# Kernel tuning notes

Measured on AMD Instinct MI355X. Metric: run time of the kernel, lower is better.

The kernel has to match this reference:

```python
import jax, jax.numpy as jnp
import numpy as np

N = 50000   # num nodes
D = 64      # feature dim
R = 4       # num relations (len(adjs))
E = 800000  # edges per relation (avg degree 16)


def setup_inputs() -> dict:
    key = jax.random.key(0)
    k0, k1, k2, k3, k4 = jax.random.split(key, 5)
    x = jax.random.normal(k0, (N, D), dtype=jnp.float32)
    weight = jax.random.normal(k1, (R,), dtype=jnp.float32)        # scalar weight per relation
    edge_vals = jax.random.uniform(k2, (R, E), dtype=jnp.float32)  # nonzero values of adjs
    edge_rows = jax.random.randint(k3, (R, E), 0, N)               # COO row (destination) indices
    edge_cols = jax.random.randint(k4, (R, E), 0, N)               # COO col (source) indices
    return {"x": x, "weight": weight, "edge_vals": edge_vals,
            "edge_rows": edge_rows, "edge_cols": edge_cols, "idx": 1}


def reference(x, weight, edge_vals, edge_rows, edge_cols, idx):
    # spmm(adjs[idx], x): gather source features, scale by edge values, scatter-add to rows
    rows = edge_rows[idx]
    cols = edge_cols[idx]
    vals = edge_vals[idx]
    msgs = vals[:, None] * x[cols]                                  # [E, D]
    agg = jax.ops.segment_sum(msgs, rows, num_segments=N)           # [N, D]
    return weight[idx] * agg
```

## Files before the change

kernel.cpp:

```cpp
#include <hip/hip_runtime.h>


#define FEAT_D 64
#define BROWS 32
#define BSH 5
#define LCAP 40
#define OVFCAP 16384
#define EPB 8192
#define BBLOCK 512
#define GBLOCK 512

__global__ void build_kernel(const float* __restrict__ edge_vals,
                             const int* __restrict__ edge_rows,
                             const int* __restrict__ edge_cols,
                             const int* __restrict__ idx_ptr,
                             int* __restrict__ bktcnt,
                             int2* __restrict__ pack,
                             int* __restrict__ ovfcnt,
                             int4* __restrict__ ovfbuf,
                             int E, int NBKT, int cap) {
    extern __shared__ int lh[];
    const long long off = (long long)idx_ptr[0] * E;
    const int* rows = edge_rows + off;
    const int* cols = edge_cols + off;
    const float* vals = edge_vals + off;
    for (int k = threadIdx.x; k < NBKT; k += blockDim.x) lh[k] = 0;
    __syncthreads();
    const int s = blockIdx.x * EPB;
    const int e2 = min(s + EPB, E);
    for (int g = s + threadIdx.x; g < e2; g += blockDim.x)
        atomicAdd(&lh[rows[g] >> BSH], 1);
    __syncthreads();
    for (int k = threadIdx.x; k < NBKT; k += blockDim.x) {
        const int c = lh[k];
        if (c) lh[k] = atomicAdd(&bktcnt[k], c);
    }
    __syncthreads();
    for (int g = s + threadIdx.x; g < e2; g += blockDim.x) {
        const int r = rows[g], c = cols[g];
        const int b = r >> BSH;
        const int pos = atomicAdd(&lh[b], 1);
        if (pos < cap) {
            pack[(long long)b * cap + pos] =
                make_int2((c << BSH) | (r & (BROWS - 1)), __float_as_int(vals[g]));
        } else {
            const int o = atomicAdd(ovfcnt, 1);
            if (o < OVFCAP) ovfbuf[o] = make_int4(r, c, __float_as_int(vals[g]), 0);
        }
    }
}

__global__ __launch_bounds__(GBLOCK) void gather_kernel(
        const float* __restrict__ x,
        const float* __restrict__ weight,
        const int* __restrict__ idx_ptr,
        const int* __restrict__ bktcnt,
        const int2* __restrict__ pack,
        int* __restrict__ ovfcnt, int4* __restrict__ ovfbuf,
        float* __restrict__ out, int N, int cap) {
    extern __shared__ int2 sh2[];
    int2* sraw = sh2;
    int2* slist = sh2 + cap;
    __shared__ int scur[32];
    const int b = blockIdx.x;
    const int t = threadIdx.x;
    const int w = t >> 6;
    const int lane = t & 63;
    if (t < 32) scur[t] = 0;
    const int cnt = min(bktcnt[b], cap);
    for (int i = t; i < cnt; i += GBLOCK)
        sraw[i] = pack[(long long)b * cap + i];
    __syncthreads();
    for (int j = lane; j < cnt; j += 64) {
        const int2 rec = sraw[j];
        const int rl = rec.x & (BROWS - 1);
        if ((rl >> 2) == w) {
            const int q = rl & 3;
            const int li = atomicAdd(&scur[w * 4 + q], 1);
            if (li < LCAP) {
                slist[(w * 4 + q) * LCAP + li] = rec;
            } else {
                const int o = atomicAdd(ovfcnt, 1);
                const int row = (b << BSH) | rl;
                if (o < OVFCAP) ovfbuf[o] = make_int4(row, rec.x >> BSH, rec.y, 0);
            }
        }
    }
    __syncthreads();
    const float wscale = weight[idx_ptr[0]];
    const int base = w * 4;
    float acc0 = 0.f, acc1 = 0.f, acc2 = 0.f, acc3 = 0.f;
#define ROWACC(Q, ACC)                                                        \
    {                                                                         \
        const int n = min(scur[base + Q], LCAP);                              \
        const int2* lp = slist + (base + Q) * LCAP;                           \
        int j = 0;                                                            \
        for (; j + 4 <= n; j += 4) {                                          \
            const int2 r0 = lp[j], r1 = lp[j + 1], r2 = lp[j + 2],            \
                       r3 = lp[j + 3];                                        \
            const float x0 = x[(r0.x >> BSH) * FEAT_D + lane];                \
            const float x1 = x[(r1.x >> BSH) * FEAT_D + lane];                \
            const float x2 = x[(r2.x >> BSH) * FEAT_D + lane];                \
            const float x3 = x[(r3.x >> BSH) * FEAT_D + lane];                \
            ACC += __int_as_float(r0.y) * x0 + __int_as_float(r1.y) * x1 +    \
                   __int_as_float(r2.y) * x2 + __int_as_float(r3.y) * x3;     \
        }                                                                     \
        for (; j < n; ++j) {                                                  \
            const int2 r0 = lp[j];                                            \
            ACC += __int_as_float(r0.y) * x[(r0.x >> BSH) * FEAT_D + lane];   \
        }                                                                     \
    }
    ROWACC(0, acc0)
    ROWACC(1, acc1)
    ROWACC(2, acc2)
    ROWACC(3, acc3)
#undef ROWACC
    const int row0 = (b << BSH) + base;
    if (row0 + 0 < N) out[(long long)(row0 + 0) * FEAT_D + lane] = wscale * acc0;
    if (row0 + 1 < N) out[(long long)(row0 + 1) * FEAT_D + lane] = wscale * acc1;
    if (row0 + 2 < N) out[(long long)(row0 + 2) * FEAT_D + lane] = wscale * acc2;
    if (row0 + 3 < N) out[(long long)(row0 + 3) * FEAT_D + lane] = wscale * acc3;
}

__global__ void fixup_kernel(const float* __restrict__ x,
                             const float* __restrict__ weight,
                             const int* __restrict__ idx_ptr,
                             const int* __restrict__ ovfcnt,
                             const int4* __restrict__ ovfbuf,
                             float* __restrict__ out) {
    const int n = min(*ovfcnt, OVFCAP);
    if (n == 0) return;
    const float ws = weight[idx_ptr[0]];
    const int gw = (int)((blockIdx.x * (long long)blockDim.x + threadIdx.x) >> 6);
    const int lane = threadIdx.x & 63;
    const int nw = (gridDim.x * blockDim.x) >> 6;
    for (int r = gw; r < n; r += nw) {
        const int4 rec = ovfbuf[r];
        atomicAdd(&out[(long long)rec.x * FEAT_D + lane],
                  ws * __int_as_float(rec.z) * x[(long long)rec.y * FEAT_D + lane]);
    }
}

__global__ void spmm_scatter_kernel(const float* __restrict__ x,
                                    const float* __restrict__ weight,
                                    const float* __restrict__ edge_vals,
                                    const int* __restrict__ edge_rows,
                                    const int* __restrict__ edge_cols,
                                    const int* __restrict__ idx_ptr,
                                    float* __restrict__ out,
                                    int E, long long work) {
    const int idx = idx_ptr[0];
    const float w = weight[idx];
    const long long rel_off = (long long)idx * E;
    long long t = (long long)blockIdx.x * blockDim.x + threadIdx.x;
    if (t >= work) return;
    const int e = (int)(t >> 4);
    const int q = (int)(t & 15);
    const int r = edge_rows[rel_off + e];
    const int c = edge_cols[rel_off + e];
    const float wv = w * edge_vals[rel_off + e];
    const float4 xv = *reinterpret_cast<const float4*>(x + (long long)c * FEAT_D + q * 4);
    float* op = out + (long long)r * FEAT_D + q * 4;
    atomicAdd(op + 0, wv * xv.x);
    atomicAdd(op + 1, wv * xv.y);
    atomicAdd(op + 2, wv * xv.z);
    atomicAdd(op + 3, wv * xv.w);
}

extern "C" void kernel_launch(void* const* d_in, const int* in_sizes, int n_in,
                              void* d_out, int out_size, void* d_ws, size_t ws_size,
                              hipStream_t stream) {
    const float* x         = (const float*)d_in[0];
    const float* weight    = (const float*)d_in[1];
    const float* edge_vals = (const float*)d_in[2];
    const int*   edge_rows = (const int*)d_in[3];
    const int*   edge_cols = (const int*)d_in[4];
    const int*   idx_ptr   = (const int*)d_in[5];
    float* out = (float*)d_out;

    const int R = in_sizes[1];
    const int E = in_sizes[2] / R;
    const int N = in_sizes[0] / FEAT_D;
    const int NBKT = (N + BROWS - 1) >> BSH;

    char* ws = (char*)d_ws;
    size_t o_bktcnt = 0;
    size_t o_ovfcnt = o_bktcnt + (size_t)NBKT * 4;
    size_t o_ovfbuf = ((o_ovfcnt + 4 + 15) / 16) * 16;
    size_t o_pack   = o_ovfbuf + (size_t)OVFCAP * 16;
    const size_t room = (ws_size > o_pack) ? (ws_size - o_pack) : 0;
    int cap = (int)(room / ((size_t)NBKT * 8));
    if (cap > 1024) cap = 1024;

    const long long meanload = (NBKT > 0) ? ((long long)E / NBKT) : 0;
    if (cap < 64 || cap < meanload + (meanload >> 3) + 16 || NBKT > 8192) {
        hipMemsetAsync(d_out, 0, (size_t)out_size * sizeof(float), stream);
        const long long work = (long long)E * 16;
        const int block = 256;
        const long long grid = (work + block - 1) / block;
        spmm_scatter_kernel<<<dim3((unsigned)grid), dim3(block), 0, stream>>>(
            x, weight, edge_vals, edge_rows, edge_cols, idx_ptr, out, E, work);
        return;
    }

    int*  bktcnt = (int*)(ws + o_bktcnt);
    int*  ovfcnt = (int*)(ws + o_ovfcnt);
    int4* ovfbuf = (int4*)(ws + o_ovfbuf);
    int2* pack   = (int2*)(ws + o_pack);

    hipMemsetAsync(bktcnt, 0, (size_t)NBKT * 4 + 4, stream);

    const int bgrid = (E + EPB - 1) / EPB;
    const size_t blds = (size_t)NBKT * 4;
    build_kernel<<<bgrid, BBLOCK, blds, stream>>>(edge_vals, edge_rows,
                                                  edge_cols, idx_ptr, bktcnt,
                                                  pack, ovfcnt, ovfbuf,
                                                  E, NBKT, cap);

    const size_t glds = ((size_t)cap + 32 * LCAP) * 8;
    gather_kernel<<<NBKT, GBLOCK, glds, stream>>>(x, weight, idx_ptr, bktcnt,
                                                  pack, ovfcnt, ovfbuf,
                                                  out, N, cap);

    fixup_kernel<<<64, 256, 0, stream>>>(x, weight, idx_ptr, ovfcnt, ovfbuf, out);
}
```

Baseline: 150.5 us.

## Bin gather-kernel edges by source-column range to improve x cache locality

Each warp's edges are now grouped by the high bits of the source column into four column ranges instead of by destination row. Each range is processed in turn with a block-wide barrier in between, so all warps touch the same slice of x at once and reuse it in cache. Rows are accumulated with predicated selects, the inner loop is unrolled to 8, and the pack loads and output stores use nontemporal hints. In exchange the kernel adds per-edge select overhead and extra barriers. It also sends N above 65536 to the fallback scatter path, and the per-list overflow cap is raised.

```diff
diff --git a/kernel.cpp b/kernel.cpp
--- a/kernel.cpp
+++ b/kernel.cpp
@@ -4,7 +4,9 @@
 #define FEAT_D 64
 #define BROWS 32
 #define BSH 5
-#define LCAP 40
+#define NCR 4
+#define CRSH 14
+#define LCAP 48
 #define OVFCAP 16384
 #define EPB 8192
 #define BBLOCK 512
@@ -61,24 +63,27 @@
     extern __shared__ int2 sh2[];
     int2* sraw = sh2;
     int2* slist = sh2 + cap;
-    __shared__ int scur[32];
+    __shared__ int scur[NCR * 8];
     const int b = blockIdx.x;
     const int t = threadIdx.x;
     const int w = t >> 6;
     const int lane = t & 63;
-    if (t < 32) scur[t] = 0;
+    if (t < NCR * 8) scur[t] = 0;
     const int cnt = min(bktcnt[b], cap);
-    for (int i = t; i < cnt; i += GBLOCK)
-        sraw[i] = pack[(long long)b * cap + i];
+    const long long* psrc = (const long long*)(pack + (long long)b * cap);
+    for (int i = t; i < cnt; i += GBLOCK) {
+        const long long raw = __builtin_nontemporal_load(psrc + i);
+        sraw[i] = make_int2((int)(unsigned)raw, (int)(raw >> 32));
+    }
     __syncthreads();
     for (int j = lane; j < cnt; j += 64) {
         const int2 rec = sraw[j];
         const int rl = rec.x & (BROWS - 1);
         if ((rl >> 2) == w) {
-            const int q = rl & 3;
-            const int li = atomicAdd(&scur[w * 4 + q], 1);
+            const int cr = rec.x >> (BSH + CRSH);
+            const int li = atomicAdd(&scur[cr * 8 + w], 1);
             if (li < LCAP) {
-                slist[(w * 4 + q) * LCAP + li] = rec;
+                slist[(cr * 8 + w) * LCAP + li] = rec;
             } else {
                 const int o = atomicAdd(ovfcnt, 1);
                 const int row = (b << BSH) | rl;
@@ -87,39 +92,62 @@
         }
     }
     __syncthreads();
-    const float wscale = weight[idx_ptr[0]];
-    const int base = w * 4;
     float acc0 = 0.f, acc1 = 0.f, acc2 = 0.f, acc3 = 0.f;
-#define ROWACC(Q, ACC)                                                        \
+#define EDGE(Rc, XV)                                                          \
     {                                                                         \
-        const int n = min(scur[base + Q], LCAP);                              \
-        const int2* lp = slist + (base + Q) * LCAP;                           \
-        int j = 0;                                                            \
-        for (; j + 4 <= n; j += 4) {                                          \
-            const int2 r0 = lp[j], r1 = lp[j + 1], r2 = lp[j + 2],            \
-                       r3 = lp[j + 3];                                        \
-            const float x0 = x[(r0.x >> BSH) * FEAT_D + lane];                \
-            const float x1 = x[(r1.x >> BSH) * FEAT_D + lane];                \
-            const float x2 = x[(r2.x >> BSH) * FEAT_D + lane];                \
-            const float x3 = x[(r3.x >> BSH) * FEAT_D + lane];                \
-            ACC += __int_as_float(r0.y) * x0 + __int_as_float(r1.y) * x1 +    \
-                   __int_as_float(r2.y) * x2 + __int_as_float(r3.y) * x3;     \
-        }                                                                     \
-        for (; j < n; ++j) {                                                  \
-            const int2 r0 = lp[j];                                            \
-            ACC += __int_as_float(r0.y) * x[(r0.x >> BSH) * FEAT_D + lane];   \
-        }                                                                     \
-    }
-    ROWACC(0, acc0)
-    ROWACC(1, acc1)
-    ROWACC(2, acc2)
-    ROWACC(3, acc3)
-#undef ROWACC
-    const int row0 = (b << BSH) + base;
-    if (row0 + 0 < N) out[(long long)(row0 + 0) * FEAT_D + lane] = wscale * acc0;
-    if (row0 + 1 < N) out[(long long)(row0 + 1) * FEAT_D + lane] = wscale * acc1;
-    if (row0 + 2 < N) out[(long long)(row0 + 2) * FEAT_D + lane] = wscale * acc2;
-    if (row0 + 3 < N) out[(long long)(row0 + 3) * FEAT_D + lane] = wscale * acc3;
+        const float m = __int_as_float(Rc.y) * XV;                            \
+        const int q = Rc.x & 3;                                               \
+        acc0 += (q == 0) ? m : 0.f;                                           \
+        acc1 += (q == 1) ? m : 0.f;                                           \
+        acc2 += (q == 2) ? m : 0.f;                                           \
+        acc3 += (q == 3) ? m : 0.f;                                           \
+    }
+    for (int cr = 0; cr < NCR; ++cr) {
+        const int li = cr * 8 + w;
+        const int n = min(scur[li], LCAP);
+        const int2* lp = slist + li * LCAP;
+        int j = 0;
+        for (; j + 8 <= n; j += 8) {
+            const int2 r0 = lp[j],     r1 = lp[j + 1], r2 = lp[j + 2],
+                       r3 = lp[j + 3], r4 = lp[j + 4], r5 = lp[j + 5],
+                       r6 = lp[j + 6], r7 = lp[j + 7];
+            const float x0 = x[(r0.x >> BSH) * FEAT_D + lane];
+            const float x1 = x[(r1.x >> BSH) * FEAT_D + lane];
+            const float x2 = x[(r2.x >> BSH) * FEAT_D + lane];
+            const float x3 = x[(r3.x >> BSH) * FEAT_D + lane];
+            const float x4 = x[(r4.x >> BSH) * FEAT_D + lane];
+            const float x5 = x[(r5.x >> BSH) * FEAT_D + lane];
+            const float x6 = x[(r6.x >> BSH) * FEAT_D + lane];
+            const float x7 = x[(r7.x >> BSH) * FEAT_D + lane];
+            EDGE(r0, x0) EDGE(r1, x1) EDGE(r2, x2) EDGE(r3, x3)
+            EDGE(r4, x4) EDGE(r5, x5) EDGE(r6, x6) EDGE(r7, x7)
+        }
+        for (; j + 4 <= n; j += 4) {
+            const int2 r0 = lp[j], r1 = lp[j + 1], r2 = lp[j + 2], r3 = lp[j + 3];
+            const float x0 = x[(r0.x >> BSH) * FEAT_D + lane];
+            const float x1 = x[(r1.x >> BSH) * FEAT_D + lane];
+            const float x2 = x[(r2.x >> BSH) * FEAT_D + lane];
+            const float x3 = x[(r3.x >> BSH) * FEAT_D + lane];
+            EDGE(r0, x0) EDGE(r1, x1) EDGE(r2, x2) EDGE(r3, x3)
+        }
+        for (; j < n; ++j) {
+            const int2 r0 = lp[j];
+            const float x0 = x[(r0.x >> BSH) * FEAT_D + lane];
+            EDGE(r0, x0)
+        }
+        __syncthreads();
+    }
+#undef EDGE
+    const float ws = weight[idx_ptr[0]];
+    const int row0 = (b << BSH) + w * 4;
+    if (row0 + 0 < N)
+        __builtin_nontemporal_store(ws * acc0, &out[(long long)(row0 + 0) * FEAT_D + lane]);
+    if (row0 + 1 < N)
+        __builtin_nontemporal_store(ws * acc1, &out[(long long)(row0 + 1) * FEAT_D + lane]);
+    if (row0 + 2 < N)
+        __builtin_nontemporal_store(ws * acc2, &out[(long long)(row0 + 2) * FEAT_D + lane]);
+    if (row0 + 3 < N)
+        __builtin_nontemporal_store(ws * acc3, &out[(long long)(row0 + 3) * FEAT_D + lane]);
 }
 
 __global__ void fixup_kernel(const float* __restrict__ x,
@@ -193,7 +221,8 @@
     if (cap > 1024) cap = 1024;
 
     const long long meanload = (NBKT > 0) ? ((long long)E / NBKT) : 0;
-    if (cap < 64 || cap < meanload + (meanload >> 3) + 16 || NBKT > 8192) {
+    if (cap < 64 || cap < meanload + (meanload >> 3) + 16 || NBKT > 8192 ||
+        N > (1 << (CRSH + 2))) {
         hipMemsetAsync(d_out, 0, (size_t)out_size * sizeof(float), stream);
         const long long work = (long long)E * 16;
         const int block = 256;
@@ -217,7 +246,7 @@
                                                   pack, ovfcnt, ovfbuf,
                                                   E, NBKT, cap);
 
-    const size_t glds = ((size_t)cap + 32 * LCAP) * 8;
+    const size_t glds = ((size_t)cap + NCR * 8 * LCAP) * 8;
     gather_kernel<<<NBKT, GBLOCK, glds, stream>>>(x, weight, idx_ptr, bktcnt,
                                                   pack, ovfcnt, ovfbuf,
                                                   out, N, cap);
```

Result: slower. 161.5 us (+7.3%).

## Stream bucket records directly into per-row lists and cache rows in build kernel

Applied to the files above, without the earlier changes.

The gather kernel no longer stages each bucket's raw records in shared memory and then rescans them per wavefront. All threads now read records once with nontemporal loads and scatter them straight into per-row lists with shared atomics. That cuts shared-memory use, drops the dynamic LDS allocation and removes one full pass over the bucket. The build kernel keeps row indices in registers between the histogram and scatter passes, halves edges per block for more blocks, and raises the per-row list cap. Output uses nontemporal stores. More contention on the per-row counters and more register pressure are the risks.

```diff
diff --git a/kernel.cpp b/kernel.cpp
--- a/kernel.cpp
+++ b/kernel.cpp
@@ -4,48 +4,64 @@
 #define FEAT_D 64
 #define BROWS 32
 #define BSH 5
-#define LCAP 40
+#define LCAP 48
 #define OVFCAP 16384
-#define EPB 8192
+#define EPB 4096
 #define BBLOCK 512
+#define EPT (EPB / BBLOCK)
 #define GBLOCK 512
 
-__global__ void build_kernel(const float* __restrict__ edge_vals,
-                             const int* __restrict__ edge_rows,
-                             const int* __restrict__ edge_cols,
-                             const int* __restrict__ idx_ptr,
-                             int* __restrict__ bktcnt,
-                             int2* __restrict__ pack,
-                             int* __restrict__ ovfcnt,
-                             int4* __restrict__ ovfbuf,
-                             int E, int NBKT, int cap) {
+__global__ __launch_bounds__(BBLOCK) void build_kernel(
+        const float* __restrict__ edge_vals,
+        const int* __restrict__ edge_rows,
+        const int* __restrict__ edge_cols,
+        const int* __restrict__ idx_ptr,
+        int* __restrict__ bktcnt,
+        int2* __restrict__ pack,
+        int* __restrict__ ovfcnt,
+        int4* __restrict__ ovfbuf,
+        int E, int NBKT, int cap) {
     extern __shared__ int lh[];
     const long long off = (long long)idx_ptr[0] * E;
     const int* rows = edge_rows + off;
     const int* cols = edge_cols + off;
     const float* vals = edge_vals + off;
-    for (int k = threadIdx.x; k < NBKT; k += blockDim.x) lh[k] = 0;
+    for (int k = threadIdx.x; k < NBKT; k += BBLOCK) lh[k] = 0;
     __syncthreads();
     const int s = blockIdx.x * EPB;
     const int e2 = min(s + EPB, E);
-    for (int g = s + threadIdx.x; g < e2; g += blockDim.x)
-        atomicAdd(&lh[rows[g] >> BSH], 1);
-    __syncthreads();
-    for (int k = threadIdx.x; k < NBKT; k += blockDim.x) {
+    int myrow[EPT];
+#pragma unroll
+    for (int k = 0; k < EPT; ++k) {
+        const int g = s + threadIdx.x + k * BBLOCK;
+        if (g < e2) {
+            const int r = rows[g];
+            myrow[k] = r;
+            atomicAdd(&lh[r >> BSH], 1);
+        }
+    }
+    __syncthreads();
+    for (int k = threadIdx.x; k < NBKT; k += BBLOCK) {
         const int c = lh[k];
         if (c) lh[k] = atomicAdd(&bktcnt[k], c);
     }
     __syncthreads();
-    for (int g = s + threadIdx.x; g < e2; g += blockDim.x) {
-        const int r = rows[g], c = cols[g];
-        const int b = r >> BSH;
-        const int pos = atomicAdd(&lh[b], 1);
-        if (pos < cap) {
-            pack[(long long)b * cap + pos] =
-                make_int2((c << BSH) | (r & (BROWS - 1)), __float_as_int(vals[g]));
-        } else {
-            const int o = atomicAdd(ovfcnt, 1);
-            if (o < OVFCAP) ovfbuf[o] = make_int4(r, c, __float_as_int(vals[g]), 0);
+#pragma unroll
+    for (int k = 0; k < EPT; ++k) {
+        const int g = s + threadIdx.x + k * BBLOCK;
+        if (g < e2) {
+            const int r = myrow[k];
+            const int b = r >> BSH;
+            const int c = cols[g];
+            const float v = vals[g];
+            const int pos = atomicAdd(&lh[b], 1);
+            if (pos < cap) {
+                pack[(long long)b * cap + pos] =
+                    make_int2((c << BSH) | (r & (BROWS - 1)), __float_as_int(v));
+            } else {
+                const int o = atomicAdd(ovfcnt, 1);
+                if (o < OVFCAP) ovfbuf[o] = make_int4(r, c, __float_as_int(v), 0);
+            }
         }
     }
 }
@@ -58,42 +74,37 @@
         const int2* __restrict__ pack,
         int* __restrict__ ovfcnt, int4* __restrict__ ovfbuf,
         float* __restrict__ out, int N, int cap) {
-    extern __shared__ int2 sh2[];
-    int2* sraw = sh2;
-    int2* slist = sh2 + cap;
-    __shared__ int scur[32];
+    __shared__ int2 slist[BROWS * LCAP];
+    __shared__ int scur[BROWS];
     const int b = blockIdx.x;
     const int t = threadIdx.x;
     const int w = t >> 6;
     const int lane = t & 63;
-    if (t < 32) scur[t] = 0;
+    if (t < BROWS) scur[t] = 0;
+    __syncthreads();
     const int cnt = min(bktcnt[b], cap);
-    for (int i = t; i < cnt; i += GBLOCK)
-        sraw[i] = pack[(long long)b * cap + i];
-    __syncthreads();
-    for (int j = lane; j < cnt; j += 64) {
-        const int2 rec = sraw[j];
+    const long long* psrc = (const long long*)(pack + (long long)b * cap);
+    for (int j = t; j < cnt; j += GBLOCK) {
+        const long long raw = __builtin_nontemporal_load(psrc + j);
+        const int2 rec = make_int2((int)(unsigned)raw, (int)(raw >> 32));
         const int rl = rec.x & (BROWS - 1);
-        if ((rl >> 2) == w) {
-            const int q = rl & 3;
-            const int li = atomicAdd(&scur[w * 4 + q], 1);
-            if (li < LCAP) {
-                slist[(w * 4 + q) * LCAP + li] = rec;
-            } else {
-                const int o = atomicAdd(ovfcnt, 1);
-                const int row = (b << BSH) | rl;
-                if (o < OVFCAP) ovfbuf[o] = make_int4(row, rec.x >> BSH, rec.y, 0);
-            }
+        const int li = atomicAdd(&scur[rl], 1);
+        if (li < LCAP) {
+            slist[rl * LCAP + li] = rec;
+        } else {
+            const int o = atomicAdd(ovfcnt, 1);
+            const int row = (b << BSH) | rl;
+            if (o < OVFCAP) ovfbuf[o] = make_int4(row, rec.x >> BSH, rec.y, 0);
         }
     }
     __syncthreads();
-    const float wscale = weight[idx_ptr[0]];
-    const int base = w * 4;
+    const float ws = weight[idx_ptr[0]];
     float acc0 = 0.f, acc1 = 0.f, acc2 = 0.f, acc3 = 0.f;
 #define ROWACC(Q, ACC)                                                        \
     {                                                                         \
-        const int n = min(scur[base + Q], LCAP);                              \
-        const int2* lp = slist + (base + Q) * LCAP;                           \
+        const int rl = w * 4 + Q;                                             \
+        const int n = min(scur[rl], LCAP);                                    \
+        const int2* lp = slist + rl * LCAP;                                   \
         int j = 0;                                                            \
         for (; j + 4 <= n; j += 4) {                                          \
             const int2 r0 = lp[j], r1 = lp[j + 1], r2 = lp[j + 2],            \
@@ -115,11 +126,15 @@
     ROWACC(2, acc2)
     ROWACC(3, acc3)
 #undef ROWACC
-    const int row0 = (b << BSH) + base;
-    if (row0 + 0 < N) out[(long long)(row0 + 0) * FEAT_D + lane] = wscale * acc0;
-    if (row0 + 1 < N) out[(long long)(row0 + 1) * FEAT_D + lane] = wscale * acc1;
-    if (row0 + 2 < N) out[(long long)(row0 + 2) * FEAT_D + lane] = wscale * acc2;
-    if (row0 + 3 < N) out[(long long)(row0 + 3) * FEAT_D + lane] = wscale * acc3;
+    const int row0 = (b << BSH) + w * 4;
+    if (row0 + 0 < N)
+        __builtin_nontemporal_store(ws * acc0, &out[(long long)(row0 + 0) * FEAT_D + lane]);
+    if (row0 + 1 < N)
+        __builtin_nontemporal_store(ws * acc1, &out[(long long)(row0 + 1) * FEAT_D + lane]);
+    if (row0 + 2 < N)
+        __builtin_nontemporal_store(ws * acc2, &out[(long long)(row0 + 2) * FEAT_D + lane]);
+    if (row0 + 3 < N)
+        __builtin_nontemporal_store(ws * acc3, &out[(long long)(row0 + 3) * FEAT_D + lane]);
 }
 
 __global__ void fixup_kernel(const float* __restrict__ x,
@@ -217,10 +232,9 @@
                                                   pack, ovfcnt, ovfbuf,
                                                   E, NBKT, cap);
 
-    const size_t glds = ((size_t)cap + 32 * LCAP) * 8;
-    gather_kernel<<<NBKT, GBLOCK, glds, stream>>>(x, weight, idx_ptr, bktcnt,
-                                                  pack, ovfcnt, ovfbuf,
-                                                  out, N, cap);
+    gather_kernel<<<NBKT, GBLOCK, 0, stream>>>(x, weight, idx_ptr, bktcnt,
+                                               pack, ovfcnt, ovfbuf,
+                                               out, N, cap);
 
     fixup_kernel<<<64, 256, 0, stream>>>(x, weight, idx_ptr, ovfcnt, ovfbuf, out);
 }
```

Result: faster. 138.8 us (-7.8%).
